# Performance work log

Hardware: AMD Instinct MI355X
Metric: run time of the kernel (lower is better)

## Reference

```python
import jax, jax.numpy as jnp
import numpy as np
from jax import lax

B_, K_, T_, V_ = 2, 4, 1024, 1024
D_MODEL, EXPAND = 512, 2
D_INNER = EXPAND * D_MODEL          # 1024
N_STATE, D_CONV, DT_RANK, L_ = 16, 4, 32, 2


def setup_inputs() -> dict:
    key = jax.random.key(0)
    ks = jax.random.split(key, 9)
    s = 0.02
    A0 = jnp.log(jnp.arange(1, N_STATE + 1, dtype=jnp.float32))  # S4D-real init
    return {
        'codes': jax.random.randint(ks[0], (B_, K_, T_), 0, V_),
        'embed_w': jax.random.normal(ks[1], (K_, V_, D_MODEL), jnp.float32) * s,
        'norm_w': jnp.ones((L_, D_MODEL), jnp.float32),
        'in_proj_w': jax.random.normal(ks[2], (L_, 2 * D_INNER, D_MODEL), jnp.float32) * s,
        'conv_w': jax.random.normal(ks[3], (L_, D_INNER, 1, D_CONV), jnp.float32) * s,
        'conv_b': jnp.zeros((L_, D_INNER), jnp.float32),
        'x_proj_w': jax.random.normal(ks[4], (L_, DT_RANK + 2 * N_STATE, D_INNER), jnp.float32) * s,
        'dt_proj_w': jax.random.normal(ks[5], (L_, D_INNER, DT_RANK), jnp.float32) * s,
        'dt_proj_b': jnp.zeros((L_, D_INNER), jnp.float32),
        'A_log': jnp.broadcast_to(A0, (L_, D_INNER, N_STATE)) + 0.0,
        'D_skip': jnp.ones((L_, D_INNER), jnp.float32),
        'out_proj_w': jax.random.normal(ks[6], (L_, D_MODEL, D_INNER), jnp.float32) * s,
        'head_w': jax.random.normal(ks[7], (K_, D_MODEL, V_), jnp.float32) * s,
    }


def rmsnorm(x, w, eps=1e-6):
    return x * w * lax.rsqrt(jnp.mean(x * x, axis=-1, keepdims=True) + eps)


def causal_dwconv(x, w, b):
    # x: (B,T,D); w: (D,1,d_conv) depthwise; torch pads d_conv-1 both sides then slices [:T]
    # == left-pad-only causal conv.
    xt = x.transpose(0, 2, 1)  # (B,D,T)
    y = lax.conv_general_dilated(xt, w, (1,), [(D_CONV - 1, 0)],
                                 feature_group_count=D_INNER,
                                 dimension_numbers=('NCH', 'OIH', 'NCH'))
    return (y + b[None, :, None]).transpose(0, 2, 1)


def mamba_block(x, norm_w, in_w, cw, cb, xp_w, dtp_w, dtp_b, A_log, D_skip, out_w):
    res = x
    x = rmsnorm(x, norm_w)
    xz = x @ in_w.T                                   # (B,T,2*d_inner)
    x_ssm, z = jnp.split(xz, 2, axis=-1)
    x_ssm = jax.nn.silu(causal_dwconv(x_ssm, cw, cb))  # (B,T,D)
    x_dbl = x_ssm @ xp_w.T                            # (B,T,dt_rank+2N)
    dt_lr, Bm, Cm = jnp.split(x_dbl, [DT_RANK, DT_RANK + N_STATE], axis=-1)
    dt = jax.nn.softplus(dt_lr @ dtp_w.T + dtp_b)     # (B,T,D)
    A = -jnp.exp(A_log)                               # (D,N)
    dA = jnp.exp(dt[..., None] * A)                   # (B,T,D,N)
    dBx = dt[..., None] * Bm[:, :, None, :] * x_ssm[..., None]  # (B,T,D,N)

    def step(h, inp):
        dA_t, dBx_t, C_t = inp
        h = dA_t * h + dBx_t                          # (B,D,N)
        return h, jnp.einsum('bdn,bn->bd', h, C_t)

    h0 = jnp.zeros((x.shape[0], D_INNER, N_STATE), x.dtype)
    _, ys = lax.scan(step, h0, (dA.transpose(1, 0, 2, 3),
                                dBx.transpose(1, 0, 2, 3),
                                Cm.transpose(1, 0, 2)))
    y = ys.transpose(1, 0, 2) + x_ssm * D_skip        # (B,T,D)
    y = y * jax.nn.silu(z)
    return res + y @ out_w.T


def reference(codes, embed_w, norm_w, in_proj_w, conv_w, conv_b, x_proj_w,
              dt_proj_w, dt_proj_b, A_log, D_skip, out_proj_w, head_w):
    k_idx = jnp.arange(K_)[None, :, None]
    x = embed_w[k_idx, codes].sum(axis=1)             # (B,T,d_model): RVQ sum-embedding
    for l in range(L_):
        x = mamba_block(x, norm_w[l], in_proj_w[l], conv_w[l], conv_b[l],
                        x_proj_w[l], dt_proj_w[l], dt_proj_b[l],
                        A_log[l], D_skip[l], out_proj_w[l])
    return jnp.einsum('btd,kdv->bktv', x, head_w)     # (B,K,T,V)
```

## Files before the change

kernel.cpp:

```cpp
#include <hip/hip_runtime.h>
#include <hip/hip_bf16.h>


#define B_SZ 2
#define K_CB 4
#define T_SZ 1024
#define V_SZ 1024
#define DM 512
#define DI 1024
#define NS 16
#define DTR 32
#define NCHUNK 64
#define TCHUNK 16

typedef unsigned short u16;
typedef long long ll;
using short8 = __attribute__((ext_vector_type(8))) short;
using f32x4  = __attribute__((ext_vector_type(4))) float;

__device__ __forceinline__ float bf2f(u16 u) {
    union { unsigned int i; float f; } v; v.i = ((unsigned int)u) << 16; return v.f;
}
__device__ __forceinline__ u16 f2bf(float f) {
    union { float f; unsigned int i; } v; v.f = f;
    unsigned int x = v.i;
    return (u16)((x + 0x7fffu + ((x >> 16) & 1u)) >> 16);
}
__device__ __forceinline__ float siluf(float x) { return x / (1.f + __expf(-x)); }
__device__ __forceinline__ float softplusf(float x) { return (x > 20.f) ? x : log1pf(__expf(x)); }

__global__ __launch_bounds__(256) void mega0_k(const float* __restrict__ in_w,
                                               const float* __restrict__ xp_w,
                                               const float* __restrict__ dtp_w,
                                               const float* __restrict__ out_w,
                                               u16* __restrict__ w_in, u16* __restrict__ w_xp,
                                               u16* __restrict__ w_dt, u16* __restrict__ w_out,
                                               const float* __restrict__ head_w,
                                               u16* __restrict__ w_hd,
                                               const int* __restrict__ codes,
                                               const float* __restrict__ ew,
                                               const float* __restrict__ nw,
                                               float* __restrict__ x,
                                               u16* __restrict__ xn) {
    __shared__ float tile[64][65];
    int bid = blockIdx.x;
    int tid = threadIdx.x;
    if (bid < 3264) {
        int i = (bid * 256 + tid) << 2;
        const float* s; u16* d;
        if (i < 2097152) { s = in_w + i; d = w_in + i; }
        else {
            i -= 2097152;
            if (i < 131072) { s = xp_w + i; d = w_xp + i; }
            else {
                i -= 131072;
                if (i < 65536) { s = dtp_w + i; d = w_dt + i; }
                else { i -= 65536; s = out_w + i; d = w_out + i; }
            }
        }
        float4 v = *(const float4*)s;
        ushort4 o; o.x = f2bf(v.x); o.y = f2bf(v.y); o.z = f2bf(v.z); o.w = f2bf(v.w);
        *(ushort4*)d = o;
    } else if (bid < 3776) {
        int idx = bid - 3264;
        int z = idx >> 7, rest = idx & 127;
        int d0 = (rest >> 4) << 6, v0 = (rest & 15) << 6;
        int col = tid & 63, rbase = tid >> 6;
#pragma unroll
        for (int i = 0; i < 16; i++) {
            int row = (i << 2) + rbase;
            tile[row][col] = head_w[(ll)z * (DM * V_SZ) + (ll)(d0 + row) * V_SZ + v0 + col];
        }
        __syncthreads();
#pragma unroll
        for (int i = 0; i < 16; i++) {
            int vrow = (i << 2) + rbase;
            w_hd[(ll)z * (V_SZ * DM) + (ll)(v0 + vrow) * DM + d0 + col] = f2bf(tile[col][vrow]);
        }
    } else {
        int row = bid - 3776;
        int b = row >> 10, t = row & 1023;
        float a0 = 0.f, a1 = 0.f;
#pragma unroll
        for (int k = 0; k < K_CB; k++) {
            int c = codes[b * (K_CB * T_SZ) + k * T_SZ + t];
            a0 += ew[((ll)k * V_SZ + c) * DM + tid];
            a1 += ew[((ll)k * V_SZ + c) * DM + tid + 256];
        }
        x[(ll)row * DM + tid]       = a0;
        x[(ll)row * DM + tid + 256] = a1;
        float ss = a0 * a0 + a1 * a1;
#pragma unroll
        for (int off = 32; off > 0; off >>= 1) ss += __shfl_down(ss, off, 64);
        float* red = &tile[0][0];
        if ((tid & 63) == 0) red[tid >> 6] = ss;
        __syncthreads();
        float tot = red[0] + red[1] + red[2] + red[3];
        float scale = rsqrtf(tot * (1.0f / DM) + 1e-6f);
        xn[(ll)row * DM + tid]       = f2bf(a0 * scale * nw[tid]);
        xn[(ll)row * DM + tid + 256] = f2bf(a1 * scale * nw[tid + 256]);
    }
}

__global__ __launch_bounds__(256) void rmsnorm_k(const float* __restrict__ x,
                                                 const float* __restrict__ w,
                                                 u16* __restrict__ xn) {
    ll row = blockIdx.x;
    const float* xr = x + row * DM;
    int tid = threadIdx.x;
    float v0 = xr[tid], v1 = xr[tid + 256];
    float ss = v0 * v0 + v1 * v1;
#pragma unroll
    for (int off = 32; off > 0; off >>= 1) ss += __shfl_down(ss, off, 64);
    __shared__ float red[4];
    if ((tid & 63) == 0) red[tid >> 6] = ss;
    __syncthreads();
    float tot = red[0] + red[1] + red[2] + red[3];
    float scale = rsqrtf(tot * (1.0f / DM) + 1e-6f);
    xn[row * DM + tid]       = f2bf(v0 * scale * w[tid]);
    xn[row * DM + tid + 256] = f2bf(v1 * scale * w[tid + 256]);
}

template <int EP>
__global__ __launch_bounds__(256) void mgemm2_k(const u16* __restrict__ A, int lda,
                                                const u16* __restrict__ W,
                                                float* __restrict__ C,
                                                u16* __restrict__ Cb, int ldcb, int K) {
    __shared__ u16 As[2][4096];
    __shared__ u16 Bs[2][4096];
    int tid = threadIdx.x;
    int wave = tid >> 6, lane = tid & 63;
    int q = lane >> 4, r = lane & 15;
    int m0 = blockIdx.y << 7, n0 = blockIdx.x << 7;
    int wm = (wave >> 1) << 6, wn = (wave & 1) << 6;
    int srow = tid >> 1, soff = (tid & 1) << 4;
    const u16* Ap = A + (ll)(m0 + srow) * lda + soff;
    const u16* Wp = W + (ll)(n0 + srow) * K + soff;
    int sidx = (srow << 5) + soff;
    f32x4 acc[4][4];
#pragma unroll
    for (int i = 0; i < 4; i++)
#pragma unroll
        for (int j = 0; j < 4; j++) acc[i][j] = (f32x4){0.f, 0.f, 0.f, 0.f};

    uint4 ra0 = *(const uint4*)Ap,       ra1 = *(const uint4*)(Ap + 8);
    uint4 rb0 = *(const uint4*)Wp,       rb1 = *(const uint4*)(Wp + 8);
    *(uint4*)&As[0][sidx] = ra0; *(uint4*)&As[0][sidx + 8] = ra1;
    *(uint4*)&Bs[0][sidx] = rb0; *(uint4*)&Bs[0][sidx + 8] = rb1;
    __syncthreads();

    int p = 0;
    for (int k0 = 0; k0 < K; k0 += 32) {
        bool pf = (k0 + 32) < K;
        if (pf) {
            ra0 = *(const uint4*)(Ap + k0 + 32); ra1 = *(const uint4*)(Ap + k0 + 40);
            rb0 = *(const uint4*)(Wp + k0 + 32); rb1 = *(const uint4*)(Wp + k0 + 40);
        }
        short8 af[4], bfr[4];
#pragma unroll
        for (int i = 0; i < 4; i++) af[i]  = *(const short8*)&As[p][((wm + (i << 4) + r) << 5) + (q << 3)];
#pragma unroll
        for (int j = 0; j < 4; j++) bfr[j] = *(const short8*)&Bs[p][((wn + (j << 4) + r) << 5) + (q << 3)];
#pragma unroll
        for (int i = 0; i < 4; i++)
#pragma unroll
            for (int j = 0; j < 4; j++)
                acc[i][j] = __builtin_amdgcn_mfma_f32_16x16x32_bf16(af[i], bfr[j], acc[i][j], 0, 0, 0);
        if (pf) {
            *(uint4*)&As[p ^ 1][sidx] = ra0; *(uint4*)&As[p ^ 1][sidx + 8] = ra1;
            *(uint4*)&Bs[p ^ 1][sidx] = rb0; *(uint4*)&Bs[p ^ 1][sidx + 8] = rb1;
        }
        __syncthreads();
        p ^= 1;
    }

#pragma unroll
    for (int i = 0; i < 4; i++)
#pragma unroll
        for (int j = 0; j < 4; j++)
#pragma unroll
            for (int g = 0; g < 4; g++) {
                int m = m0 + wm + (i << 4) + (q << 2) + g;
                int n = n0 + wn + (j << 4) + r;
                float v = acc[i][j][g];
                if (EP == 0) {
                    Cb[(ll)m * ldcb + n] = f2bf(v);
                } else {
                    int z = n >> 10, vv = n & 1023;
                    int b = m >> 10, t = m & 1023;
                    C[((ll)(b * K_CB + z) * T_SZ + t) * V_SZ + vv] = v;
                }
            }
}

template <int EP>
__global__ __launch_bounds__(256) void mgemm_k(const u16* __restrict__ A, int lda,
                                               const u16* __restrict__ W,
                                               float* __restrict__ C, int ldc, int K,
                                               const float* __restrict__ bias,
                                               u16* __restrict__ Cb, int ldcb) {
    __shared__ u16 As[2][2048];
    __shared__ u16 Bs[2][2048];
    int tid = threadIdx.x;
    int m0 = blockIdx.y << 6, n0 = blockIdx.x << 6;
    int lane = tid & 63, wave = tid >> 6;
    int q = lane >> 4, r = lane & 15;
    int wm = (wave >> 1) << 5, wn = (wave & 1) << 5;
    int srow = tid >> 2, soff = (tid & 3) << 3;
    const u16* Ap = A + (ll)(m0 + srow) * lda + soff;
    const u16* Wp = W + (ll)(n0 + srow) * K + soff;
    int sidx = (srow << 5) + soff;
    f32x4 acc[2][2];
#pragma unroll
    for (int i = 0; i < 2; i++)
#pragma unroll
        for (int j = 0; j < 2; j++) acc[i][j] = (f32x4){0.f, 0.f, 0.f, 0.f};

    uint4 ra = *(const uint4*)Ap;
    uint4 rb = *(const uint4*)Wp;
    *(uint4*)&As[0][sidx] = ra;
    *(uint4*)&Bs[0][sidx] = rb;
    __syncthreads();

    int p = 0;
    for (int k0 = 0; k0 < K; k0 += 32) {
        bool pf = (k0 + 32) < K;
        if (pf) {
            ra = *(const uint4*)(Ap + k0 + 32);
            rb = *(const uint4*)(Wp + k0 + 32);
        }
        short8 af[2], bfr[2];
#pragma unroll
        for (int i = 0; i < 2; i++) af[i]  = *(const short8*)&As[p][((wm + (i << 4) + r) << 5) + (q << 3)];
#pragma unroll
        for (int j = 0; j < 2; j++) bfr[j] = *(const short8*)&Bs[p][((wn + (j << 4) + r) << 5) + (q << 3)];
#pragma unroll
        for (int i = 0; i < 2; i++)
#pragma unroll
            for (int j = 0; j < 2; j++)
                acc[i][j] = __builtin_amdgcn_mfma_f32_16x16x32_bf16(af[i], bfr[j], acc[i][j], 0, 0, 0);
        if (pf) {
            *(uint4*)&As[p ^ 1][sidx] = ra;
            *(uint4*)&Bs[p ^ 1][sidx] = rb;
        }
        __syncthreads();
        p ^= 1;
    }

#pragma unroll
    for (int i = 0; i < 2; i++)
#pragma unroll
        for (int j = 0; j < 2; j++)
#pragma unroll
            for (int g = 0; g < 4; g++) {
                int m = m0 + wm + (i << 4) + (q << 2) + g;
                int n = n0 + wn + (j << 4) + r;
                float v = acc[i][j][g];
                if (EP == 1) {
                    C[(ll)m * ldc + n] = v;
                    Cb[(ll)m * ldcb + n] = f2bf(v);
                } else {
                    float nv = C[(ll)m * ldc + n] + v;
                    C[(ll)m * ldc + n] = nv;
                    Cb[(ll)m * ldcb + n] = f2bf(nv);
                }
            }
}

__global__ __launch_bounds__(256) void conv_k(const u16* __restrict__ xzb,
                                              const float* __restrict__ cw,
                                              const float* __restrict__ cb,
                                              float* __restrict__ xc,
                                              u16* __restrict__ xcb) {
    int row = blockIdx.x;
    int b = row >> 10, t = row & 1023;
    int c0 = threadIdx.x << 2;
    float4 a = *(const float4*)&cb[c0];
    float acc[4] = {a.x, a.y, a.z, a.w};
    float4 cwv[4];
#pragma unroll
    for (int e = 0; e < 4; e++) cwv[e] = *(const float4*)&cw[(c0 + e) << 2];
#pragma unroll
    for (int j = 0; j < 4; j++) {
        int tt = t - 3 + j;
        if (tt >= 0) {
            ushort4 v = *(const ushort4*)&xzb[((ll)(b * T_SZ + tt)) * (2 * DI) + c0];
            acc[0] = fmaf(bf2f(v.x), ((const float*)&cwv[0])[j], acc[0]);
            acc[1] = fmaf(bf2f(v.y), ((const float*)&cwv[1])[j], acc[1]);
            acc[2] = fmaf(bf2f(v.z), ((const float*)&cwv[2])[j], acc[2]);
            acc[3] = fmaf(bf2f(v.w), ((const float*)&cwv[3])[j], acc[3]);
        }
    }
    float4 s; ushort4 sb;
    s.x = siluf(acc[0]); s.y = siluf(acc[1]); s.z = siluf(acc[2]); s.w = siluf(acc[3]);
    sb.x = f2bf(s.x); sb.y = f2bf(s.y); sb.z = f2bf(s.z); sb.w = f2bf(s.w);
    *(float4*)&xc[(ll)row * DI + c0] = s;
    *(ushort4*)&xcb[(ll)row * DI + c0] = sb;
}

__global__ __launch_bounds__(256) void dtscan1_k(const u16* __restrict__ A,
                                                 const u16* __restrict__ W,
                                                 const float* __restrict__ bias,
                                                 const float* __restrict__ xc,
                                                 const float* __restrict__ xdbl,
                                                 const float* __restrict__ A_log,
                                                 float* __restrict__ dtb,
                                                 float* __restrict__ pA,
                                                 float* __restrict__ U) {
    __shared__ u16 As[2048];
    __shared__ u16 Bs[2048];
    __shared__ float dts[64][65];
    __shared__ float BCs[64][16];
    int tid = threadIdx.x;
    int m0 = blockIdx.y << 6, n0 = blockIdx.x << 6;
    int lane = tid & 63, wave = tid >> 6;
    int q = lane >> 4, r = lane & 15;
    int wm = (wave >> 1) << 5, wn = (wave & 1) << 5;
    {
        int srow = tid >> 2, soff = (tid & 3) << 3;
        *(uint4*)&As[(srow << 5) + soff] = *(const uint4*)(A + (ll)(m0 + srow) * 64 + soff);
        *(uint4*)&Bs[(srow << 5) + soff] = *(const uint4*)(W + (ll)(n0 + srow) * DTR + soff);
        int rr = tid >> 2, cc = (tid & 3) << 2;
        *(float4*)&BCs[rr][cc] = *(const float4*)&xdbl[(ll)(m0 + rr) * 64 + DTR + cc];
    }
    int sd = lane;
    int sc = wave;
    int dg = n0 + sd;
    float Av[NS];
#pragma unroll
    for (int n4 = 0; n4 < 4; n4++) {
        float4 alv = *(const float4*)&A_log[dg * NS + (n4 << 2)];
        Av[(n4 << 2) + 0] = -__expf(alv.x); Av[(n4 << 2) + 1] = -__expf(alv.y);
        Av[(n4 << 2) + 2] = -__expf(alv.z); Av[(n4 << 2) + 3] = -__expf(alv.w);
    }
    __syncthreads();

    f32x4 acc[2][2];
#pragma unroll
    for (int i = 0; i < 2; i++)
#pragma unroll
        for (int j = 0; j < 2; j++) acc[i][j] = (f32x4){0.f, 0.f, 0.f, 0.f};
    short8 af[2], bfr[2];
#pragma unroll
    for (int i = 0; i < 2; i++) af[i]  = *(const short8*)&As[((wm + (i << 4) + r) << 5) + (q << 3)];
#pragma unroll
    for (int j = 0; j < 2; j++) bfr[j] = *(const short8*)&Bs[((wn + (j << 4) + r) << 5) + (q << 3)];
#pragma unroll
    for (int i = 0; i < 2; i++)
#pragma unroll
        for (int j = 0; j < 2; j++)
            acc[i][j] = __builtin_amdgcn_mfma_f32_16x16x32_bf16(af[i], bfr[j], acc[i][j], 0, 0, 0);

#pragma unroll
    for (int i = 0; i < 2; i++)
#pragma unroll
        for (int j = 0; j < 2; j++)
#pragma unroll
            for (int g = 0; g < 4; g++) {
                int mm = wm + (i << 4) + (q << 2) + g;
                int nn = wn + (j << 4) + r;
                float dtl = softplusf(acc[i][j][g] + bias[n0 + nn]);
                dtb[(ll)(m0 + mm) * DI + (n0 + nn)] = dtl;
                dts[mm][nn] = dtl;
            }
    __syncthreads();

    int b = m0 >> 10;
    int c = ((m0 & 1023) >> 4) + sc;
    int tl0 = sc << 4;
    float p[NS], u[NS];
#pragma unroll
    for (int n = 0; n < NS; n++) { p[n] = 1.f; u[n] = 0.f; }
#pragma unroll
    for (int s = 0; s < TCHUNK; s++) {
        int tl = tl0 + s;
        float dtv = dts[tl][sd];
        float xv = xc[(ll)(m0 + tl) * DI + dg];
        float dx = dtv * xv;
#pragma unroll
        for (int n = 0; n < NS; n++) {
            float aa = __expf(dtv * Av[n]);
            p[n] *= aa;
            u[n] = fmaf(aa, u[n], dx * BCs[tl][n]);
        }
    }
    ll o = (((ll)b * NCHUNK + c) * DI + dg) * NS;
#pragma unroll
    for (int n = 0; n < NS; n++) { pA[o + n] = p[n]; U[o + n] = u[n]; }
}

__global__ __launch_bounds__(256) void scan2_k(const float* __restrict__ pA,
                                               const float* __restrict__ U,
                                               float* __restrict__ hst) {
    int i = blockIdx.x * 256 + threadIdx.x;
    int b = i >> 14;
    int rest = i & 16383;
    float h = 0.f;
#pragma unroll
    for (int c = 0; c < NCHUNK; c++) {
        ll o = ((ll)b * NCHUNK + c) * (DI * NS) + rest;
        float pa = pA[o], u = U[o];
        hst[o] = h;
        h = fmaf(pa, h, u);
    }
}

__global__ __launch_bounds__(256) void scan3_k(const float* __restrict__ dt,
                                               const float* __restrict__ xc,
                                               const float* __restrict__ xdbl,
                                               const u16* __restrict__ xzb,
                                               const float* __restrict__ A_log,
                                               const float* __restrict__ Dk,
                                               const float* __restrict__ hst,
                                               u16* __restrict__ y) {
    int blk = blockIdx.x;
    int dblk = blk & 3;
    int c = (blk >> 2) & (NCHUNK - 1);
    int b = blk >> 8;
    int d = dblk * 256 + threadIdx.x;
    int t0 = c * TCHUNK;
    __shared__ float BC[TCHUNK][32];
    if (threadIdx.x < TCHUNK * 8) {
        int rr = threadIdx.x >> 3, cc = (threadIdx.x & 7) << 2;
        *(float4*)&BC[rr][cc] = *(const float4*)&xdbl[((ll)(b * T_SZ + t0 + rr)) * 64 + DTR + cc];
    }
    float Av[NS];
#pragma unroll
    for (int n4 = 0; n4 < 4; n4++) {
        float4 alv = *(const float4*)&A_log[d * NS + (n4 << 2)];
        Av[(n4 << 2) + 0] = -__expf(alv.x); Av[(n4 << 2) + 1] = -__expf(alv.y);
        Av[(n4 << 2) + 2] = -__expf(alv.z); Av[(n4 << 2) + 3] = -__expf(alv.w);
    }
    float h[NS];
    ll ho = (((ll)b * NCHUNK + c) * DI + d) * NS;
#pragma unroll
    for (int n = 0; n < NS; n++) h[n] = hst[ho + n];
    float Dv = Dk[d];
    __syncthreads();
#pragma unroll
    for (int s = 0; s < TCHUNK; s++) {
        ll ro = (ll)(b * T_SZ + t0 + s);
        float dtv = dt[ro * DI + d];
        float xv = xc[ro * DI + d];
        float dx = dtv * xv;
        float acc = 0.f;
#pragma unroll
        for (int n = 0; n < NS; n++) {
            float aa = __expf(dtv * Av[n]);
            h[n] = fmaf(aa, h[n], dx * BC[s][n]);
            acc = fmaf(h[n], BC[s][16 + n], acc);
        }
        float zv = bf2f(xzb[ro * (2 * DI) + DI + d]);
        y[ro * DI + d] = f2bf((acc + xv * Dv) * siluf(zv));
    }
}

extern "C" void kernel_launch(void* const* d_in, const int* in_sizes, int n_in,
                              void* d_out, int out_size, void* d_ws, size_t ws_size,
                              hipStream_t stream) {
    const int*   codes   = (const int*)d_in[0];
    const float* embed_w = (const float*)d_in[1];
    const float* norm_w  = (const float*)d_in[2];
    const float* in_w    = (const float*)d_in[3];
    const float* conv_w  = (const float*)d_in[4];
    const float* conv_b  = (const float*)d_in[5];
    const float* xp_w    = (const float*)d_in[6];
    const float* dtp_w   = (const float*)d_in[7];
    const float* dtp_b   = (const float*)d_in[8];
    const float* A_log   = (const float*)d_in[9];
    const float* D_skip  = (const float*)d_in[10];
    const float* out_w   = (const float*)d_in[11];
    const float* head_w  = (const float*)d_in[12];
    float* out = (float*)d_out;

    float* ws = (float*)d_ws;
    float* x    = ws;
    float* xc   = x + 1048576;
    float* dtb  = xc + 2097152;
    float* xdbl = dtb + 2097152;
    float* pA   = xdbl + 131072;
    float* Uh   = pA + 2097152;

    u16* us       = (u16*)(Uh + 2097152);
    u16* xz_bf    = us;
    u16* xc_bf    = xz_bf + 4194304;
    u16* ybxn_bf  = xc_bf + 2097152;
    u16* xdbl_bf  = ybxn_bf + 2097152;
    u16* w_in_bf  = xdbl_bf + 131072;
    u16* w_xp_bf  = w_in_bf + 2097152;
    u16* w_dt_bf  = w_xp_bf + 131072;
    u16* w_out_bf = w_dt_bf + 65536;
    u16* w_hd_bf  = w_out_bf + 1048576;

    u16* xn_bf = ybxn_bf;
    u16* y_bf  = ybxn_bf;
    u16* x_bf  = xc_bf;

    mega0_k<<<5824, 256, 0, stream>>>(in_w, xp_w, dtp_w, out_w,
                                      w_in_bf, w_xp_bf, w_dt_bf, w_out_bf,
                                      head_w, w_hd_bf, codes, embed_w, norm_w, x, xn_bf);

    for (int l = 0; l < 2; l++) {
        const float* al = A_log + l * DI * NS;
        if (l == 1)
            rmsnorm_k<<<2048, 256, 0, stream>>>(x, norm_w + DM, xn_bf);
        mgemm2_k<0><<<dim3(16, 16), 256, 0, stream>>>(xn_bf, DM, w_in_bf + l * 1048576,
                                                      nullptr, xz_bf, 2 * DI, DM);
        conv_k<<<2048, 256, 0, stream>>>(xz_bf, conv_w + l * DI * 4, conv_b + l * DI, xc, xc_bf);
        mgemm_k<1><<<dim3(1, 32), 256, 0, stream>>>(xc_bf, DI, w_xp_bf + l * 65536,
                                                    xdbl, 64, DI, nullptr, xdbl_bf, 64);
        dtscan1_k<<<dim3(16, 32), 256, 0, stream>>>(xdbl_bf, w_dt_bf + l * 32768,
                                                    dtp_b + l * DI, xc, xdbl, al,
                                                    dtb, pA, Uh);
        scan2_k<<<128, 256, 0, stream>>>(pA, Uh, Uh);
        scan3_k<<<512, 256, 0, stream>>>(dtb, xc, xdbl, xz_bf, al, D_skip + l * DI, Uh, y_bf);
        mgemm_k<3><<<dim3(8, 32), 256, 0, stream>>>(y_bf, DI, w_out_bf + l * 524288,
                                                    x, DM, DI, nullptr, x_bf, DM);
    }

    mgemm2_k<4><<<dim3(32, 16), 256, 0, stream>>>(x_bf, DM, w_hd_bf, out, nullptr, 0, DM);
}
```

Baseline: 302.9 us.

## Fuse causal depthwise conv with x_proj GEMM in one kernel

Replaces the separate conv kernel and the x_proj GEMM launch with one kernel. Each block computes the conv and SiLU for 16 timesteps across all 1024 channels, keeps the bf16 result in shared memory, and runs the 16x64 x_proj MFMA GEMM directly from it. This removes the bf16 xc round trip through global memory and one launch, and reuses loaded xz rows across neighbouring timesteps. The cost is only 128 blocks, and each walks the full K=1024 reduction serially with a barrier every step, which may leave much of the GPU idle.

```diff
diff --git a/kernel.cpp b/kernel.cpp
--- a/kernel.cpp
+++ b/kernel.cpp
@@ -256,46 +256,82 @@
                 int m = m0 + wm + (i << 4) + (q << 2) + g;
                 int n = n0 + wn + (j << 4) + r;
                 float v = acc[i][j][g];
-                if (EP == 1) {
-                    C[(ll)m * ldc + n] = v;
-                    Cb[(ll)m * ldcb + n] = f2bf(v);
-                } else {
-                    float nv = C[(ll)m * ldc + n] + v;
-                    C[(ll)m * ldc + n] = nv;
-                    Cb[(ll)m * ldcb + n] = f2bf(nv);
-                }
+                float nv = C[(ll)m * ldc + n] + v;
+                C[(ll)m * ldc + n] = nv;
+                Cb[(ll)m * ldcb + n] = f2bf(nv);
             }
 }
 
-__global__ __launch_bounds__(256) void conv_k(const u16* __restrict__ xzb,
-                                              const float* __restrict__ cw,
-                                              const float* __restrict__ cb,
-                                              float* __restrict__ xc,
-                                              u16* __restrict__ xcb) {
-    int row = blockIdx.x;
-    int b = row >> 10, t = row & 1023;
-    int c0 = threadIdx.x << 2;
+__global__ __launch_bounds__(256) void convxp_k(const u16* __restrict__ xzb,
+                                                const float* __restrict__ cw,
+                                                const float* __restrict__ cb,
+                                                const u16* __restrict__ W,
+                                                float* __restrict__ xc,
+                                                float* __restrict__ xdbl,
+                                                u16* __restrict__ xdbl_bf) {
+    __shared__ u16 xcs[16][1032];
+    __shared__ u16 Bs[2][2048];
+    int blk = blockIdx.x, tid = threadIdx.x;
+    int b = blk >> 6, tg = blk & 63;
+    int t0 = tg << 4;
+    ll ro0 = (ll)b * T_SZ + t0;
+    int c0 = tid << 2;
     float4 a = *(const float4*)&cb[c0];
-    float acc[4] = {a.x, a.y, a.z, a.w};
     float4 cwv[4];
 #pragma unroll
     for (int e = 0; e < 4; e++) cwv[e] = *(const float4*)&cw[(c0 + e) << 2];
-#pragma unroll
-    for (int j = 0; j < 4; j++) {
-        int tt = t - 3 + j;
-        if (tt >= 0) {
-            ushort4 v = *(const ushort4*)&xzb[((ll)(b * T_SZ + tt)) * (2 * DI) + c0];
-            acc[0] = fmaf(bf2f(v.x), ((const float*)&cwv[0])[j], acc[0]);
-            acc[1] = fmaf(bf2f(v.y), ((const float*)&cwv[1])[j], acc[1]);
-            acc[2] = fmaf(bf2f(v.z), ((const float*)&cwv[2])[j], acc[2]);
-            acc[3] = fmaf(bf2f(v.w), ((const float*)&cwv[3])[j], acc[3]);
-        }
-    }
-    float4 s; ushort4 sb;
-    s.x = siluf(acc[0]); s.y = siluf(acc[1]); s.z = siluf(acc[2]); s.w = siluf(acc[3]);
-    sb.x = f2bf(s.x); sb.y = f2bf(s.y); sb.z = f2bf(s.z); sb.w = f2bf(s.w);
-    *(float4*)&xc[(ll)row * DI + c0] = s;
-    *(ushort4*)&xcb[(ll)row * DI + c0] = sb;
+    ushort4 v[19];
+#pragma unroll
+    for (int i = 0; i < 19; i++) {
+        int t = t0 - 3 + i;
+        if (t >= 0) v[i] = *(const ushort4*)&xzb[((ll)(b * T_SZ + t)) * (2 * DI) + c0];
+        else        v[i] = (ushort4){0, 0, 0, 0};
+    }
+#pragma unroll
+    for (int tr = 0; tr < 16; tr++) {
+        float acc0 = a.x, acc1 = a.y, acc2 = a.z, acc3 = a.w;
+#pragma unroll
+        for (int j = 0; j < 4; j++) {
+            ushort4 vv = v[tr + j];
+            acc0 = fmaf(bf2f(vv.x), ((const float*)&cwv[0])[j], acc0);
+            acc1 = fmaf(bf2f(vv.y), ((const float*)&cwv[1])[j], acc1);
+            acc2 = fmaf(bf2f(vv.z), ((const float*)&cwv[2])[j], acc2);
+            acc3 = fmaf(bf2f(vv.w), ((const float*)&cwv[3])[j], acc3);
+        }
+        float4 s; ushort4 sb;
+        s.x = siluf(acc0); s.y = siluf(acc1); s.z = siluf(acc2); s.w = siluf(acc3);
+        sb.x = f2bf(s.x); sb.y = f2bf(s.y); sb.z = f2bf(s.z); sb.w = f2bf(s.w);
+        *(float4*)&xc[(ro0 + tr) * DI + c0] = s;
+        *(ushort4*)&xcs[tr][c0] = sb;
+    }
+    __syncthreads();
+
+    int lane = tid & 63, wave = tid >> 6;
+    int q = lane >> 4, r = lane & 15;
+    int srow = tid >> 2, soff = (tid & 3) << 3;
+    f32x4 acc = (f32x4){0.f, 0.f, 0.f, 0.f};
+    uint4 rb = *(const uint4*)(W + (ll)srow * DI + soff);
+    *(uint4*)&Bs[0][(srow << 5) + soff] = rb;
+    __syncthreads();
+    int p = 0;
+    for (int k0 = 0; k0 < DI; k0 += 32) {
+        bool pf = (k0 + 32) < DI;
+        if (pf) rb = *(const uint4*)(W + (ll)srow * DI + k0 + 32 + soff);
+        short8 af  = *(const short8*)&xcs[r][k0 + (q << 3)];
+        short8 bfr = *(const short8*)&Bs[p][(((wave << 4) + r) << 5) + (q << 3)];
+        acc = __builtin_amdgcn_mfma_f32_16x16x32_bf16(af, bfr, acc, 0, 0, 0);
+        if (pf) *(uint4*)&Bs[p ^ 1][(srow << 5) + soff] = rb;
+        __syncthreads();
+        p ^= 1;
+    }
+#pragma unroll
+    for (int g = 0; g < 4; g++) {
+        int tr = (q << 2) + g;
+        int n = (wave << 4) + r;
+        float vv = acc[g];
+        xdbl[(ro0 + tr) * 64 + n]    = vv;
+        xdbl_bf[(ro0 + tr) * 64 + n] = f2bf(vv);
+    }
 }
 
 __global__ __launch_bounds__(256) void dtscan1_k(const u16* __restrict__ A,
@@ -483,8 +519,8 @@
 
     u16* us       = (u16*)(Uh + 2097152);
     u16* xz_bf    = us;
-    u16* xc_bf    = xz_bf + 4194304;
-    u16* ybxn_bf  = xc_bf + 2097152;
+    u16* xbf      = xz_bf + 4194304;
+    u16* ybxn_bf  = xbf + 2097152;
     u16* xdbl_bf  = ybxn_bf + 2097152;
     u16* w_in_bf  = xdbl_bf + 131072;
     u16* w_xp_bf  = w_in_bf + 2097152;
@@ -494,7 +530,7 @@
 
     u16* xn_bf = ybxn_bf;
     u16* y_bf  = ybxn_bf;
-    u16* x_bf  = xc_bf;
+    u16* x_bf  = xbf;
 
     mega0_k<<<5824, 256, 0, stream>>>(in_w, xp_w, dtp_w, out_w,
                                       w_in_bf, w_xp_bf, w_dt_bf, w_out_bf,
@@ -506,9 +542,8 @@
             rmsnorm_k<<<2048, 256, 0, stream>>>(x, norm_w + DM, xn_bf);
         mgemm2_k<0><<<dim3(16, 16), 256, 0, stream>>>(xn_bf, DM, w_in_bf + l * 1048576,
                                                       nullptr, xz_bf, 2 * DI, DM);
-        conv_k<<<2048, 256, 0, stream>>>(xz_bf, conv_w + l * DI * 4, conv_b + l * DI, xc, xc_bf);
-        mgemm_k<1><<<dim3(1, 32), 256, 0, stream>>>(xc_bf, DI, w_xp_bf + l * 65536,
-                                                    xdbl, 64, DI, nullptr, xdbl_bf, 64);
+        convxp_k<<<128, 256, 0, stream>>>(xz_bf, conv_w + l * DI * 4, conv_b + l * DI,
+                                          w_xp_bf + l * 65536, xc, xdbl, xdbl_bf);
         dtscan1_k<<<dim3(16, 32), 256, 0, stream>>>(xdbl_bf, w_dt_bf + l * 32768,
                                                     dtp_b + l * DI, xc, xdbl, al,
                                                     dtb, pA, Uh);
```

Result: faster. 284.3 us (-6.1%).
